# Optimization experiments

Measured on AMD Instinct MI355X. Metric: run time of the kernel, lower is better.

## Reference

```python
import jax, jax.numpy as jnp
import numpy as np

EUCLTHRES = 0.02  # module default, meters
N_VERTS = 10475   # SMPL-X vertex count
BATCH = 2


def setup_inputs() -> dict:
    key = jax.random.key(0)
    k1, k2 = jax.random.split(key)
    vertices = jax.random.normal(k1, (BATCH, N_VERTS, 3), dtype=jnp.float32)
    # geodesic mask: True where geodesic distance >= geothres (most pairs)
    geomask = jax.random.randint(k2, (N_VERTS, N_VERTS), 0, 2) > 0
    # symmetrize like a real geodesic-distance-derived mask
    geomask = jnp.logical_or(geomask, geomask.T)
    return {"vertices": vertices, "geomask": geomask}


def reference(vertices, geomask):
    # batch_pairwise_dist (squared): ||x_i||^2 + ||x_j||^2 - 2 x_i . x_j
    sq = jnp.sum(vertices * vertices, axis=-1)                      # [B, N]
    dots = jnp.einsum('bnd,bmd->bnm', vertices, vertices)           # [B, N, N]
    v2v = sq[:, :, None] + sq[:, None, :] - 2.0 * dots              # [B, N, N]
    # v2v[:, ~geomask] = inf  (mask out geodesically-close pairs)
    v2v = jnp.where(geomask[None, :, :], v2v, jnp.inf)
    # torch.min(v2v, dim=1): min over first vertex index for each column j
    v2v_min = jnp.min(v2v, axis=1)                                  # [B, N]
    in_contact = v2v_min < EUCLTHRES ** 2                           # [B, N] bool
    return (v2v_min, in_contact)
```

## Files before the change

### kernel.cpp

```cpp
#include <hip/hip_runtime.h>
#include <math.h>


#define NV   10475
#define NB   2
#define BLK  256
#define CPB  1024
#define JB   ((NV + CPB - 1) / CPB)
#define RC   128
#define CH   ((NV + RC - 1) / RC)
#define RU   4

__device__ __forceinline__ float sq_nofma(float x, float y, float z) {
    return __fadd_rn(__fadd_rn(__fmul_rn(x, x), __fmul_rn(y, y)), __fmul_rn(z, z));
}

__global__ __launch_bounds__(BLK) void sc_partial(
    const float* __restrict__ verts,
    const int*   __restrict__ gmask,
    float*       __restrict__ partial)
{
    __shared__ float4 sv[CH * NB];

    const int tid = threadIdx.x;
    const int jb  = blockIdx.x;
    const int rc  = blockIdx.y;
    const int r0  = rc * CH;
    const int r1  = (r0 + CH < NV) ? (r0 + CH) : NV;
    const int nrows = r1 - r0;

    for (int k = tid; k < nrows * NB; k += BLK) {
        int rr = k >> 1, b = k & 1;
        const float* vp = verts + ((size_t)b * NV + (r0 + rr)) * 3;
        float x = vp[0], y = vp[1], z = vp[2];
        sv[rr * NB + b] = make_float4(x, y, z, sq_nofma(x, y, z));
    }
    __syncthreads();

    int  cols[4];
    bool cval[4];
    float cx[NB][4], cy[NB][4], cz[NB][4], cs[NB][4];
#pragma unroll
    for (int c = 0; c < 4; ++c) {
        int col = jb * CPB + tid + c * BLK;
        cval[c] = (col < NV);
        cols[c] = cval[c] ? col : (NV - 1);
#pragma unroll
        for (int b = 0; b < NB; ++b) {
            const float* vp = verts + ((size_t)b * NV + cols[c]) * 3;
            float x = vp[0], y = vp[1], z = vp[2];
            cx[b][c] = x; cy[b][c] = y; cz[b][c] = z;
            cs[b][c] = sq_nofma(x, y, z);
        }
    }

    float mn[NB][4];
#pragma unroll
    for (int b = 0; b < NB; ++b)
#pragma unroll
        for (int c = 0; c < 4; ++c) mn[b][c] = __builtin_inff();

    int i = r0;
    for (; i + RU <= r1; i += RU) {
        int mk[RU][4];
#pragma unroll
        for (int r = 0; r < RU; ++r) {
            const int* grow = gmask + (size_t)(i + r) * NV;
#pragma unroll
            for (int c = 0; c < 4; ++c) mk[r][c] = grow[cols[c]];
        }
#pragma unroll
        for (int r = 0; r < RU; ++r) {
            float4 a0 = sv[(i - r0 + r) * NB + 0];
            float4 a1 = sv[(i - r0 + r) * NB + 1];
#pragma unroll
            for (int c = 0; c < 4; ++c) {
                bool act = cval[c] && (mk[r][c] != 0);

                float d0 = __fadd_rn(__fadd_rn(__fmul_rn(a0.x, cx[0][c]),
                                               __fmul_rn(a0.y, cy[0][c])),
                                     __fmul_rn(a0.z, cz[0][c]));
                float v0 = __fsub_rn(__fadd_rn(a0.w, cs[0][c]), 2.0f * d0);
                mn[0][c] = fminf(mn[0][c], act ? v0 : __builtin_inff());

                float d1 = __fadd_rn(__fadd_rn(__fmul_rn(a1.x, cx[1][c]),
                                               __fmul_rn(a1.y, cy[1][c])),
                                     __fmul_rn(a1.z, cz[1][c]));
                float v1 = __fsub_rn(__fadd_rn(a1.w, cs[1][c]), 2.0f * d1);
                mn[1][c] = fminf(mn[1][c], act ? v1 : __builtin_inff());
            }
        }
    }
    for (; i < r1; ++i) {
        const int* grow = gmask + (size_t)i * NV;
        float4 a0 = sv[(i - r0) * NB + 0];
        float4 a1 = sv[(i - r0) * NB + 1];
#pragma unroll
        for (int c = 0; c < 4; ++c) {
            bool act = cval[c] && (grow[cols[c]] != 0);

            float d0 = __fadd_rn(__fadd_rn(__fmul_rn(a0.x, cx[0][c]),
                                           __fmul_rn(a0.y, cy[0][c])),
                                 __fmul_rn(a0.z, cz[0][c]));
            float v0 = __fsub_rn(__fadd_rn(a0.w, cs[0][c]), 2.0f * d0);
            mn[0][c] = fminf(mn[0][c], act ? v0 : __builtin_inff());

            float d1 = __fadd_rn(__fadd_rn(__fmul_rn(a1.x, cx[1][c]),
                                           __fmul_rn(a1.y, cy[1][c])),
                                 __fmul_rn(a1.z, cz[1][c]));
            float v1 = __fsub_rn(__fadd_rn(a1.w, cs[1][c]), 2.0f * d1);
            mn[1][c] = fminf(mn[1][c], act ? v1 : __builtin_inff());
        }
    }

#pragma unroll
    for (int c = 0; c < 4; ++c) {
        if (cval[c]) {
            size_t base = (size_t)rc * (NB * NV);
            partial[base + 0 * NV + cols[c]] = mn[0][c];
            partial[base + 1 * NV + cols[c]] = mn[1][c];
        }
    }
}

__global__ __launch_bounds__(BLK) void sc_reduce(
    const float* __restrict__ partial,
    float*       __restrict__ out)
{
    int idx = blockIdx.x * BLK + threadIdx.x;
    if (idx >= NB * NV) return;
    float m = __builtin_inff();
#pragma unroll 8
    for (int r = 0; r < RC; ++r)
        m = fminf(m, partial[(size_t)r * (NB * NV) + idx]);
    out[idx] = m;
    out[NB * NV + idx] = ((double)m < 0.02 * 0.02) ? 1.0f : 0.0f;
}

extern "C" void kernel_launch(void* const* d_in, const int* in_sizes, int n_in,
                              void* d_out, int out_size, void* d_ws, size_t ws_size,
                              hipStream_t stream) {
    const float* verts = (const float*)d_in[0];
    const int*   gmask = (const int*)d_in[1];
    float* out     = (float*)d_out;
    float* partial = (float*)d_ws;

    dim3 g1(JB, RC);
    sc_partial<<<g1, dim3(BLK), 0, stream>>>(verts, gmask, partial);

    int nred = (NB * NV + BLK - 1) / BLK;
    sc_reduce<<<nred, dim3(BLK), 0, stream>>>(partial, out);
}
```

Measured before the change: 609.9 us.

## Exploit pairwise-distance symmetry to compute only the lower block triangle

Each column block now processes only the rows up to its last column index, skipping the upper block triangle. The skipped entries are recovered by also reducing each row across the wave with DPP min operations and writing row-wise partial minima. The reduce kernel then combines column partials with the row partials from later column blocks. Pre-doubling the column coordinates also removes the per-pair multiply by two. The shortcut assumes the geodesic mask is symmetric, which the input construction guarantees, and it adds per-row cross-lane reduction and extra partial writes.

```diff
diff --git a/kernel.cpp b/kernel.cpp
--- a/kernel.cpp
+++ b/kernel.cpp
@@ -7,27 +7,50 @@
 #define BLK  256
 #define CPB  1024
 #define JB   ((NV + CPB - 1) / CPB)
-#define RC   128
-#define CH   ((NV + RC - 1) / RC)
+#define CH   48
+#define RC   ((NV + CH - 1) / CH)
 #define RU   4
 
 __device__ __forceinline__ float sq_nofma(float x, float y, float z) {
     return __fadd_rn(__fadd_rn(__fmul_rn(x, x), __fmul_rn(y, y)), __fmul_rn(z, z));
 }
 
+template <int CTRL>
+__device__ __forceinline__ float dppmin(float v) {
+    int s = __builtin_amdgcn_update_dpp(__float_as_int(v), __float_as_int(v),
+                                        CTRL, 0xF, 0xF, false);
+    return fminf(v, __int_as_float(s));
+}
+
+__device__ __forceinline__ float wave_min_to_lane63(float v) {
+    v = dppmin<0x111>(v);
+    v = dppmin<0x112>(v);
+    v = dppmin<0x114>(v);
+    v = dppmin<0x118>(v);
+    v = dppmin<0x142>(v);
+    v = dppmin<0x143>(v);
+    return v;
+}
+
 __global__ __launch_bounds__(BLK) void sc_partial(
     const float* __restrict__ verts,
     const int*   __restrict__ gmask,
-    float*       __restrict__ partial)
+    float*       __restrict__ colpart,
+    float*       __restrict__ rowpart)
 {
     __shared__ float4 sv[CH * NB];
+    __shared__ float  rmin[CH][4][NB];
 
-    const int tid = threadIdx.x;
-    const int jb  = blockIdx.x;
-    const int rc  = blockIdx.y;
-    const int r0  = rc * CH;
-    const int r1  = (r0 + CH < NV) ? (r0 + CH) : NV;
+    const int tid  = threadIdx.x;
+    const int jb   = blockIdx.x;
+    const int rcb  = blockIdx.y;
+    const int j0   = jb * CPB;
+    const int jmax = (j0 + CPB - 1 < NV - 1) ? (j0 + CPB - 1) : (NV - 1);
+    const int r0   = rcb * CH;
+    if (r0 > jmax) return;
+    const int r1    = ((r0 + CH < jmax + 1) ? (r0 + CH) : (jmax + 1));
     const int nrows = r1 - r0;
+    const int wv    = tid >> 6;
 
     for (int k = tid; k < nrows * NB; k += BLK) {
         int rr = k >> 1, b = k & 1;
@@ -39,18 +62,20 @@
 
     int  cols[4];
     bool cval[4];
-    float cx[NB][4], cy[NB][4], cz[NB][4], cs[NB][4];
+    float cx2[NB][4], cy2[NB][4], cz2[NB][4], cs[NB][4];
 #pragma unroll
     for (int c = 0; c < 4; ++c) {
-        int col = jb * CPB + tid + c * BLK;
+        int col = j0 + tid + c * BLK;
         cval[c] = (col < NV);
         cols[c] = cval[c] ? col : (NV - 1);
 #pragma unroll
         for (int b = 0; b < NB; ++b) {
             const float* vp = verts + ((size_t)b * NV + cols[c]) * 3;
             float x = vp[0], y = vp[1], z = vp[2];
-            cx[b][c] = x; cy[b][c] = y; cz[b][c] = z;
-            cs[b][c] = sq_nofma(x, y, z);
+            cx2[b][c] = __fmul_rn(2.0f, x);
+            cy2[b][c] = __fmul_rn(2.0f, y);
+            cz2[b][c] = __fmul_rn(2.0f, z);
+            cs[b][c]  = sq_nofma(x, y, z);
         }
     }
 
@@ -59,6 +84,39 @@
     for (int b = 0; b < NB; ++b)
 #pragma unroll
         for (int c = 0; c < 4; ++c) mn[b][c] = __builtin_inff();
+
+#define ROW_BODY(ROWIDX, MK0, MK1, MK2, MK3)                                   \
+    {                                                                          \
+        int rr = (ROWIDX);                                                     \
+        float4 a0 = sv[rr * NB + 0];                                           \
+        float4 a1 = sv[rr * NB + 1];                                           \
+        float rf0 = __builtin_inff(), rf1 = __builtin_inff();                  \
+        int mks[4] = {MK0, MK1, MK2, MK3};                                     \
+        _Pragma("unroll")                                                      \
+        for (int c = 0; c < 4; ++c) {                                          \
+            bool act = cval[c] && (mks[c] != 0);                               \
+            float d0 = __fadd_rn(__fadd_rn(__fmul_rn(a0.x, cx2[0][c]),         \
+                                           __fmul_rn(a0.y, cy2[0][c])),        \
+                                 __fmul_rn(a0.z, cz2[0][c]));                  \
+            float v0 = __fsub_rn(__fadd_rn(a0.w, cs[0][c]), d0);               \
+            float t0 = act ? v0 : __builtin_inff();                            \
+            mn[0][c] = fminf(mn[0][c], t0);                                    \
+            rf0      = fminf(rf0, t0);                                         \
+            float d1 = __fadd_rn(__fadd_rn(__fmul_rn(a1.x, cx2[1][c]),         \
+                                           __fmul_rn(a1.y, cy2[1][c])),        \
+                                 __fmul_rn(a1.z, cz2[1][c]));                  \
+            float v1 = __fsub_rn(__fadd_rn(a1.w, cs[1][c]), d1);               \
+            float t1 = act ? v1 : __builtin_inff();                            \
+            mn[1][c] = fminf(mn[1][c], t1);                                    \
+            rf1      = fminf(rf1, t1);                                         \
+        }                                                                      \
+        rf0 = wave_min_to_lane63(rf0);                                         \
+        rf1 = wave_min_to_lane63(rf1);                                         \
+        if ((tid & 63) == 63) {                                                \
+            rmin[rr][wv][0] = rf0;                                             \
+            rmin[rr][wv][1] = rf1;                                             \
+        }                                                                      \
+    }
 
     int i = r0;
     for (; i + RU <= r1; i += RU) {
@@ -70,69 +128,56 @@
             for (int c = 0; c < 4; ++c) mk[r][c] = grow[cols[c]];
         }
 #pragma unroll
-        for (int r = 0; r < RU; ++r) {
-            float4 a0 = sv[(i - r0 + r) * NB + 0];
-            float4 a1 = sv[(i - r0 + r) * NB + 1];
-#pragma unroll
-            for (int c = 0; c < 4; ++c) {
-                bool act = cval[c] && (mk[r][c] != 0);
-
-                float d0 = __fadd_rn(__fadd_rn(__fmul_rn(a0.x, cx[0][c]),
-                                               __fmul_rn(a0.y, cy[0][c])),
-                                     __fmul_rn(a0.z, cz[0][c]));
-                float v0 = __fsub_rn(__fadd_rn(a0.w, cs[0][c]), 2.0f * d0);
-                mn[0][c] = fminf(mn[0][c], act ? v0 : __builtin_inff());
-
-                float d1 = __fadd_rn(__fadd_rn(__fmul_rn(a1.x, cx[1][c]),
-                                               __fmul_rn(a1.y, cy[1][c])),
-                                     __fmul_rn(a1.z, cz[1][c]));
-                float v1 = __fsub_rn(__fadd_rn(a1.w, cs[1][c]), 2.0f * d1);
-                mn[1][c] = fminf(mn[1][c], act ? v1 : __builtin_inff());
-            }
-        }
+        for (int r = 0; r < RU; ++r)
+            ROW_BODY(i - r0 + r, mk[r][0], mk[r][1], mk[r][2], mk[r][3]);
     }
     for (; i < r1; ++i) {
         const int* grow = gmask + (size_t)i * NV;
-        float4 a0 = sv[(i - r0) * NB + 0];
-        float4 a1 = sv[(i - r0) * NB + 1];
-#pragma unroll
-        for (int c = 0; c < 4; ++c) {
-            bool act = cval[c] && (grow[cols[c]] != 0);
+        int m0 = grow[cols[0]], m1 = grow[cols[1]];
+        int m2 = grow[cols[2]], m3 = grow[cols[3]];
+        ROW_BODY(i - r0, m0, m1, m2, m3);
+    }
+#undef ROW_BODY
 
-            float d0 = __fadd_rn(__fadd_rn(__fmul_rn(a0.x, cx[0][c]),
-                                           __fmul_rn(a0.y, cy[0][c])),
-                                 __fmul_rn(a0.z, cz[0][c]));
-            float v0 = __fsub_rn(__fadd_rn(a0.w, cs[0][c]), 2.0f * d0);
-            mn[0][c] = fminf(mn[0][c], act ? v0 : __builtin_inff());
+    __syncthreads();
 
-            float d1 = __fadd_rn(__fadd_rn(__fmul_rn(a1.x, cx[1][c]),
-                                           __fmul_rn(a1.y, cy[1][c])),
-                                 __fmul_rn(a1.z, cz[1][c]));
-            float v1 = __fsub_rn(__fadd_rn(a1.w, cs[1][c]), 2.0f * d1);
-            mn[1][c] = fminf(mn[1][c], act ? v1 : __builtin_inff());
-        }
+    for (int k = tid; k < nrows * NB; k += BLK) {
+        int rr = k >> 1, b = k & 1;
+        float m = fminf(fminf(rmin[rr][0][b], rmin[rr][1][b]),
+                        fminf(rmin[rr][2][b], rmin[rr][3][b]));
+        rowpart[((size_t)jb * NB + b) * NV + (r0 + rr)] = m;
     }
 
 #pragma unroll
     for (int c = 0; c < 4; ++c) {
         if (cval[c]) {
-            size_t base = (size_t)rc * (NB * NV);
-            partial[base + 0 * NV + cols[c]] = mn[0][c];
-            partial[base + 1 * NV + cols[c]] = mn[1][c];
+            colpart[((size_t)rcb * NB + 0) * NV + cols[c]] = mn[0][c];
+            colpart[((size_t)rcb * NB + 1) * NV + cols[c]] = mn[1][c];
         }
     }
 }
 
 __global__ __launch_bounds__(BLK) void sc_reduce(
-    const float* __restrict__ partial,
+    const float* __restrict__ colpart,
+    const float* __restrict__ rowpart,
     float*       __restrict__ out)
 {
     int idx = blockIdx.x * BLK + threadIdx.x;
     if (idx >= NB * NV) return;
+    int b = idx / NV, j = idx - b * NV;
+
+    int jb    = j / CPB;
+    int jmax  = ((jb + 1) * CPB - 1 < NV - 1) ? ((jb + 1) * CPB - 1) : (NV - 1);
+    int rcmax = jmax / CH;
+
     float m = __builtin_inff();
-#pragma unroll 8
-    for (int r = 0; r < RC; ++r)
-        m = fminf(m, partial[(size_t)r * (NB * NV) + idx]);
+    for (int rcb = 0; rcb <= rcmax; ++rcb)
+        m = fminf(m, colpart[((size_t)rcb * NB + b) * NV + j]);
+#pragma unroll
+    for (int jb2 = 0; jb2 < JB; ++jb2)
+        if (jb2 >= jb)
+            m = fminf(m, rowpart[((size_t)jb2 * NB + b) * NV + j]);
+
     out[idx] = m;
     out[NB * NV + idx] = ((double)m < 0.02 * 0.02) ? 1.0f : 0.0f;
 }
@@ -143,11 +188,12 @@
     const float* verts = (const float*)d_in[0];
     const int*   gmask = (const int*)d_in[1];
     float* out     = (float*)d_out;
-    float* partial = (float*)d_ws;
+    float* colpart = (float*)d_ws;
+    float* rowpart = colpart + (size_t)RC * NB * NV;
 
     dim3 g1(JB, RC);
-    sc_partial<<<g1, dim3(BLK), 0, stream>>>(verts, gmask, partial);
+    sc_partial<<<g1, dim3(BLK), 0, stream>>>(verts, gmask, colpart, rowpart);
 
     int nred = (NB * NV + BLK - 1) / BLK;
-    sc_reduce<<<nred, dim3(BLK), 0, stream>>>(partial, out);
+    sc_reduce<<<nred, dim3(BLK), 0, stream>>>(colpart, rowpart, out);
 }
```

Result: faster. 591.4 us (-3.0%).
